# Optimization experiments

Hardware: AMD Instinct MI355X
Metric: run time of the kernel (lower is better)

Reference implementation:

```python
import jax, jax.numpy as jnp
import numpy as np

N_NODES = 100000
N_EDGES = 1000000
D_FEAT = 64


def setup_inputs() -> dict:
    key = jax.random.key(0)
    k1, k2 = jax.random.split(key)
    x = jax.random.normal(k1, (N_NODES, D_FEAT), dtype=jnp.float32)
    edge_index = jax.random.randint(k2, (2, N_EDGES), 0, N_NODES, dtype=jnp.int64)
    return {"x": x, "edge_index": edge_index}


def reference(x, edge_index):
    # message: x_j = x[edge_index[1]]  (per-edge gather)
    # aggregate: scatter_add into destination nodes edge_index[0], dim_size = N
    # update: identity
    msg = x[edge_index[1]]                                  # [E, d]
    out = jax.ops.segment_sum(msg, edge_index[0], num_segments=x.shape[0])  # [N, d]
    return out
```

## Files before the change

### kernel.cpp

```cpp
#include <hip/hip_runtime.h>

#define D_FEAT     64
#define CSHIFT     8
#define CNODES     256
#define MAXC       512
#define CCAP       3072
#define CNT_STRIDE 16
#define PACK_SHIFT 24
#define PSRC_MASK  ((1 << PACK_SHIFT) - 1)
#define P_BLOCK    512
#define P_EPT      4
#define PB_EDGES   (P_BLOCK * P_EPT)
#define A_BLOCK    512
#define HCAP       2048

__global__ __launch_bounds__(256) void mp_scatter_kernel(
    const float* __restrict__ x,
    const int* __restrict__ ei,
    float* __restrict__ out,
    int E) {
    long long tid = (long long)blockIdx.x * blockDim.x + threadIdx.x;
    int e = (int)(tid >> 6);
    int f = (int)(tid & 63);
    if (e >= E) return;
    int dst = ei[e];
    int src = ei[E + e];
    float v = x[(long long)src * D_FEAT + f];
    unsafeAtomicAdd(&out[(long long)dst * D_FEAT + f], v);
}

__global__ __launch_bounds__(P_BLOCK) void partition_edges(
    const int* __restrict__ ei, int E, int nbins,
    int* __restrict__ binCount,
    int* __restrict__ binList) {
    __shared__ int  hist[MAXC];
    __shared__ int  loff[MAXC];
    __shared__ int  gbase[MAXC];
    __shared__ int  cur[MAXC];
    __shared__ int2 sOut[PB_EDGES];

    int t = threadIdx.x;
    for (int b = t; b < nbins; b += P_BLOCK) hist[b] = 0;

    int start = blockIdx.x * PB_EDGES;
    int ecnt = E - start; if (ecnt > PB_EDGES) ecnt = PB_EDGES;

    int dk[P_EPT], sk[P_EPT];
    bool vec = (ecnt == PB_EDGES) && ((E & 3) == 0);
    if (vec) {
        int4 d4 = ((const int4*)(ei + start))[t];
        int4 s4 = ((const int4*)(ei + E + start))[t];
        dk[0] = d4.x; dk[1] = d4.y; dk[2] = d4.z; dk[3] = d4.w;
        sk[0] = s4.x; sk[1] = s4.y; sk[2] = s4.z; sk[3] = s4.w;
    } else {
#pragma unroll
        for (int k = 0; k < P_EPT; ++k) {
            int i = t * P_EPT + k;
            dk[k] = (i < ecnt) ? ei[start + i] : 0;
            sk[k] = (i < ecnt) ? ei[E + start + i] : 0;
        }
    }
    __syncthreads();

#pragma unroll
    for (int k = 0; k < P_EPT; ++k) {
        int i = t * P_EPT + k;
        if (i < ecnt) atomicAdd(&hist[dk[k] >> CSHIFT], 1);
    }
    __syncthreads();

    if (t < 64) {
        int chunk = (nbins + 63) >> 6;
        int base_i = t * chunk;
        int vals[8];
        int sum = 0;
        for (int k = 0; k < chunk; ++k) {
            int b = base_i + k;
            vals[k] = (b < nbins) ? hist[b] : 0;
            sum += vals[k];
        }
        int inc = sum;
#pragma unroll
        for (int d = 1; d < 64; d <<= 1) {
            int y = __shfl_up(inc, d, 64);
            if (t >= d) inc += y;
        }
        int excl = inc - sum;
        for (int k = 0; k < chunk; ++k) {
            int b = base_i + k;
            if (b < nbins) { loff[b] = excl; cur[b] = excl; excl += vals[k]; }
        }
    }
    __syncthreads();

    for (int b = t; b < nbins; b += P_BLOCK) {
        int h = hist[b];
        if (h) gbase[b] = atomicAdd(&binCount[b * CNT_STRIDE], h);
    }
    __syncthreads();

#pragma unroll
    for (int k = 0; k < P_EPT; ++k) {
        int i = t * P_EPT + k;
        if (i < ecnt) {
            int dst = dk[k];
            int b = dst >> CSHIFT;
            int r = atomicAdd(&cur[b], 1);
            int gpos = gbase[b] + (r - loff[b]);
            int slot = (gpos < CCAP) ? (b * CCAP + gpos) : -1;
            sOut[r] = make_int2(slot,
                                (int)(((unsigned)(dst & (CNODES - 1)) << PACK_SHIFT) |
                                      (unsigned)sk[k]));
        }
    }
    __syncthreads();

    for (int i = t; i < ecnt; i += P_BLOCK) {
        int2 o = sOut[i];
        if (o.x >= 0) binList[o.x] = o.y;
    }
}

__global__ __launch_bounds__(A_BLOCK, 6) void bin_accumulate(
    const float* __restrict__ x,
    const int* __restrict__ binCount,
    const int* __restrict__ binList,
    float* __restrict__ out,
    int N) {
    __shared__ int sList[CCAP];
    __shared__ int sCsr[HCAP];
    __shared__ int sCnt[128];
    __shared__ int sOff[128];
    __shared__ int sRank[128];

    int coarse = blockIdx.x >> 1;
    int half   = blockIdx.x & 1;
    int t = threadIdx.x;

    int cnt = binCount[coarse * CNT_STRIDE];
    if (cnt > CCAP) cnt = CCAP;

    if (t < 128) sCnt[t] = 0;
    __syncthreads();

    const int4* bl4 = (const int4*)(binList + coarse * CCAP);
    int nvec = (cnt + 3) >> 2;
    for (int v = t; v < nvec; v += A_BLOCK) {
        int4 e4 = bl4[v];
        ((int4*)sList)[v] = e4;
        int pk[4] = {e4.x, e4.y, e4.z, e4.w};
        int i = v << 2;
#pragma unroll
        for (int j = 0; j < 4; ++j) {
            if (i + j < cnt) {
                unsigned ld = ((unsigned)pk[j]) >> PACK_SHIFT;
                if ((int)(ld >> 7) == half) atomicAdd(&sCnt[ld & 127], 1);
            }
        }
    }
    __syncthreads();

    if (t < 64) {
        int c0 = sCnt[2 * t];
        int c1 = sCnt[2 * t + 1];
        int sum = c0 + c1;
        int inc = sum;
#pragma unroll
        for (int d = 1; d < 64; d <<= 1) {
            int y = __shfl_up(inc, d, 64);
            if (t >= d) inc += y;
        }
        int excl = inc - sum;
        sOff[2 * t]     = excl;      sRank[2 * t]     = excl;
        sOff[2 * t + 1] = excl + c0; sRank[2 * t + 1] = excl + c0;
    }
    __syncthreads();

    for (int i = t; i < cnt; i += A_BLOCK) {
        int p = sList[i];
        unsigned ld = ((unsigned)p) >> PACK_SHIFT;
        if ((int)(ld >> 7) == half) {
            int r = atomicAdd(&sRank[ld & 127], 1);
            if (r < HCAP) sCsr[r] = p & PSRC_MASK;
        }
    }
    __syncthreads();

    int wave = t >> 6;
    int lane = t & 63;
    int q    = lane >> 4;
    int sub  = lane & 15;

    int nodeBase = (coarse << CSHIFT) + (half << 7);
    int nodesInH = N - nodeBase; if (nodesInH > 128) nodesInH = 128;

    for (int n0 = wave; n0 < nodesInH; n0 += 16) {
        int n1 = n0 + 8;
        int hasB = (n1 < nodesInH);

        int offA = sOff[n0];
        int degA = sCnt[n0];
        if (offA + degA > HCAP) degA = (HCAP > offA) ? (HCAP - offA) : 0;
        int offB = 0, degB = 0;
        if (hasB) {
            offB = sOff[n1];
            degB = sCnt[n1];
            if (offB + degB > HCAP) degB = (HCAP > offB) ? (HCAP - offB) : 0;
        }

        float4 accA = make_float4(0.f, 0.f, 0.f, 0.f);
        float4 accB = make_float4(0.f, 0.f, 0.f, 0.f);
        int dmax = degA > degB ? degA : degB;

        for (int e0 = 0; e0 < dmax; e0 += 16) {
            float4 vA[4], vB[4];
#pragma unroll
            for (int j = 0; j < 4; ++j) {
                int eidx = e0 + j * 4 + q;
                vA[j] = make_float4(0.f, 0.f, 0.f, 0.f);
                if (eidx < degA) {
                    int s = sCsr[offA + eidx];
                    vA[j] = ((const float4*)(x + (long long)s * D_FEAT))[sub];
                }
            }
#pragma unroll
            for (int j = 0; j < 4; ++j) {
                int eidx = e0 + j * 4 + q;
                vB[j] = make_float4(0.f, 0.f, 0.f, 0.f);
                if (eidx < degB) {
                    int s = sCsr[offB + eidx];
                    vB[j] = ((const float4*)(x + (long long)s * D_FEAT))[sub];
                }
            }
#pragma unroll
            for (int j = 0; j < 4; ++j) {
                accA.x += vA[j].x; accA.y += vA[j].y;
                accA.z += vA[j].z; accA.w += vA[j].w;
                accB.x += vB[j].x; accB.y += vB[j].y;
                accB.z += vB[j].z; accB.w += vB[j].w;
            }
        }

        accA.x += __shfl_xor(accA.x, 16, 64);
        accA.y += __shfl_xor(accA.y, 16, 64);
        accA.z += __shfl_xor(accA.z, 16, 64);
        accA.w += __shfl_xor(accA.w, 16, 64);
        accA.x += __shfl_xor(accA.x, 32, 64);
        accA.y += __shfl_xor(accA.y, 32, 64);
        accA.z += __shfl_xor(accA.z, 32, 64);
        accA.w += __shfl_xor(accA.w, 32, 64);

        accB.x += __shfl_xor(accB.x, 16, 64);
        accB.y += __shfl_xor(accB.y, 16, 64);
        accB.z += __shfl_xor(accB.z, 16, 64);
        accB.w += __shfl_xor(accB.w, 16, 64);
        accB.x += __shfl_xor(accB.x, 32, 64);
        accB.y += __shfl_xor(accB.y, 32, 64);
        accB.z += __shfl_xor(accB.z, 32, 64);
        accB.w += __shfl_xor(accB.w, 32, 64);

        if (q == 0) {
            ((float4*)(out + (long long)(nodeBase + n0) * D_FEAT))[sub] = accA;
            if (hasB)
                ((float4*)(out + (long long)(nodeBase + n1) * D_FEAT))[sub] = accB;
        }
    }
}

extern "C" void kernel_launch(void* const* d_in, const int* in_sizes, int n_in,
                              void* d_out, int out_size, void* d_ws, size_t ws_size,
                              hipStream_t stream) {
    const float* x   = (const float*)d_in[0];
    const int*   ei  = (const int*)d_in[1];
    float*       out = (float*)d_out;

    int E = in_sizes[1] / 2;
    int N = out_size / D_FEAT;
    int nbins = (N + CNODES - 1) >> CSHIFT;

    size_t list_bytes  = (size_t)nbins * CCAP * sizeof(int);
    size_t count_bytes = (size_t)nbins * CNT_STRIDE * sizeof(int);
    size_t need = list_bytes + count_bytes;

    if (nbins > MAXC || N > (1 << PACK_SHIFT) || ws_size < need) {
        hipMemsetAsync(out, 0, (size_t)out_size * sizeof(float), stream);
        long long total = (long long)E * D_FEAT;
        int block = 256;
        int grid = (int)((total + block - 1) / block);
        mp_scatter_kernel<<<grid, block, 0, stream>>>(x, ei, out, E);
        return;
    }

    int* binList  = (int*)d_ws;
    int* binCount = (int*)((char*)d_ws + list_bytes);

    hipMemsetAsync(binCount, 0, count_bytes, stream);

    {
        int grid = (E + PB_EDGES - 1) / PB_EDGES;
        partition_edges<<<grid, P_BLOCK, 0, stream>>>(ei, E, nbins, binCount, binList);
    }
    {
        bin_accumulate<<<nbins * 2, A_BLOCK, 0, stream>>>(x, binCount, binList, out, N);
    }
}
```

Measured before the change: 133.2 us.

## Make gathers unconditional with masked accumulate, double edges per partition thread

The accumulate loop now loads all source indices first and issues every feature gather unconditionally. Masked-off lanes read row sCsr[0], and a 0/1 multiplier zeroes them in the sum. This removes divergent branches and lets all loads be in flight together. Separately, the partition kernel processes 8 edges per thread with two int4 loads each, which halves the block count. The accumulate kernel's min-blocks hint drops from 6 to 4 to give it more registers. Extra wasted gathers on tail iterations and a NaN/Inf multiplied by zero in x[sCsr[0]] could corrupt results. The larger partition block also raises shared memory use (sOut doubles to 32KB).

Result: faster. 129.4 us (-2.8%).

```diff
diff --git a/kernel.cpp b/kernel.cpp
--- a/kernel.cpp
+++ b/kernel.cpp
@@ -9,7 +9,7 @@
 #define PACK_SHIFT 24
 #define PSRC_MASK  ((1 << PACK_SHIFT) - 1)
 #define P_BLOCK    512
-#define P_EPT      4
+#define P_EPT      8
 #define PB_EDGES   (P_BLOCK * P_EPT)
 #define A_BLOCK    512
 #define HCAP       2048
@@ -48,10 +48,14 @@
     int dk[P_EPT], sk[P_EPT];
     bool vec = (ecnt == PB_EDGES) && ((E & 3) == 0);
     if (vec) {
-        int4 d4 = ((const int4*)(ei + start))[t];
-        int4 s4 = ((const int4*)(ei + E + start))[t];
-        dk[0] = d4.x; dk[1] = d4.y; dk[2] = d4.z; dk[3] = d4.w;
-        sk[0] = s4.x; sk[1] = s4.y; sk[2] = s4.z; sk[3] = s4.w;
+        int4 d0 = ((const int4*)(ei + start))[2 * t];
+        int4 d1 = ((const int4*)(ei + start))[2 * t + 1];
+        int4 s0 = ((const int4*)(ei + E + start))[2 * t];
+        int4 s1 = ((const int4*)(ei + E + start))[2 * t + 1];
+        dk[0] = d0.x; dk[1] = d0.y; dk[2] = d0.z; dk[3] = d0.w;
+        dk[4] = d1.x; dk[5] = d1.y; dk[6] = d1.z; dk[7] = d1.w;
+        sk[0] = s0.x; sk[1] = s0.y; sk[2] = s0.z; sk[3] = s0.w;
+        sk[4] = s1.x; sk[5] = s1.y; sk[6] = s1.z; sk[7] = s1.w;
     } else {
 #pragma unroll
         for (int k = 0; k < P_EPT; ++k) {
@@ -121,7 +125,7 @@
     }
 }
 
-__global__ __launch_bounds__(A_BLOCK, 6) void bin_accumulate(
+__global__ __launch_bounds__(A_BLOCK, 4) void bin_accumulate(
     const float* __restrict__ x,
     const int* __restrict__ binCount,
     const int* __restrict__ binList,
@@ -213,31 +217,31 @@
         int dmax = degA > degB ? degA : degB;
 
         for (int e0 = 0; e0 < dmax; e0 += 16) {
+            bool mA[4], mB[4];
+            int  sAi[4], sBi[4];
+#pragma unroll
+            for (int j = 0; j < 4; ++j) {
+                int e = e0 + j * 4 + q;
+                mA[j] = (e < degA);
+                mB[j] = (e < degB);
+                sAi[j] = sCsr[mA[j] ? (offA + e) : 0];
+                sBi[j] = sCsr[mB[j] ? (offB + e) : 0];
+            }
             float4 vA[4], vB[4];
 #pragma unroll
+            for (int j = 0; j < 4; ++j)
+                vA[j] = ((const float4*)(x + (long long)sAi[j] * D_FEAT))[sub];
+#pragma unroll
+            for (int j = 0; j < 4; ++j)
+                vB[j] = ((const float4*)(x + (long long)sBi[j] * D_FEAT))[sub];
+#pragma unroll
             for (int j = 0; j < 4; ++j) {
-                int eidx = e0 + j * 4 + q;
-                vA[j] = make_float4(0.f, 0.f, 0.f, 0.f);
-                if (eidx < degA) {
-                    int s = sCsr[offA + eidx];
-                    vA[j] = ((const float4*)(x + (long long)s * D_FEAT))[sub];
-                }
-            }
-#pragma unroll
-            for (int j = 0; j < 4; ++j) {
-                int eidx = e0 + j * 4 + q;
-                vB[j] = make_float4(0.f, 0.f, 0.f, 0.f);
-                if (eidx < degB) {
-                    int s = sCsr[offB + eidx];
-                    vB[j] = ((const float4*)(x + (long long)s * D_FEAT))[sub];
-                }
-            }
-#pragma unroll
-            for (int j = 0; j < 4; ++j) {
-                accA.x += vA[j].x; accA.y += vA[j].y;
-                accA.z += vA[j].z; accA.w += vA[j].w;
-                accB.x += vB[j].x; accB.y += vB[j].y;
-                accB.z += vB[j].z; accB.w += vB[j].w;
+                float fa = mA[j] ? 1.f : 0.f;
+                float fb = mB[j] ? 1.f : 0.f;
+                accA.x += fa * vA[j].x; accA.y += fa * vA[j].y;
+                accA.z += fa * vA[j].z; accA.w += fa * vA[j].w;
+                accB.x += fb * vB[j].x; accB.y += fb * vB[j].y;
+                accB.z += fb * vB[j].z; accB.w += fb * vB[j].w;
             }
         }
 
```
